# Kernel tuning notes

Measured on AMD Instinct MI355X. Metric: run time of the kernel, lower is better.

Reference implementation:

```python
import jax, jax.numpy as jnp
import numpy as np

B, I_LEN, Q_LEN, H = 256, 256, 64, 512
MID, G, FLAT_OUT = 512, 1, 1024


def setup_inputs() -> dict:
    key = jax.random.key(0)
    ks = jax.random.split(key, 20)
    s = lambda k, sh: jax.random.normal(k, sh, dtype=jnp.float32) * 0.02
    inp = {
        'i_batch': jax.random.normal(ks[0], (B, I_LEN, H), dtype=jnp.float32),
        'q_batch': jax.random.normal(ks[1], (B, Q_LEN, H), dtype=jnp.float32),
        'i_mask': jax.random.bernoulli(ks[2], 0.1, (B, 1, 1, I_LEN)),
        'q_mask': jax.random.bernoulli(ks[3], 0.1, (B, 1, 1, Q_LEN)),
        # l_flatten (applied to i_feat) params
        'lf_w1': s(ks[4], (H, MID)), 'lf_b1': jnp.zeros((MID,), jnp.float32),
        'lf_w2': s(ks[5], (MID, G)), 'lf_b2': jnp.zeros((G,), jnp.float32),
        'lf_wm': s(ks[6], (H * G, FLAT_OUT)), 'lf_bm': jnp.zeros((FLAT_OUT,), jnp.float32),
        # i_flatten (applied to l_feat) params
        'if_w1': s(ks[7], (H, MID)), 'if_b1': jnp.zeros((MID,), jnp.float32),
        'if_w2': s(ks[8], (MID, G)), 'if_b2': jnp.zeros((G,), jnp.float32),
        'if_wm': s(ks[9], (H * G, FLAT_OUT)), 'if_bm': jnp.zeros((FLAT_OUT,), jnp.float32),
        # fh_h: Linear(1024, 512)
        'fh_w': s(ks[10], (FLAT_OUT, 512)), 'fh_b': jnp.zeros((512,), jnp.float32),
    }
    return inp


def _qkv_attention(query, key, value, mask):
    # query [B,Lq,H], key/value [B,Lk,H], mask [B,1,1,Lk] (True = pad)
    d_k = query.shape[-1]
    scores = jnp.einsum('bqh,bkh->bqk', query, key) / jnp.sqrt(jnp.asarray(d_k, query.dtype))
    scores = jnp.where(mask[:, 0], jnp.asarray(-65504.0, scores.dtype), scores)
    p_attn = jax.nn.softmax(scores, axis=-1)
    return jnp.einsum('bqk,bkh->bqh', p_attn, value)


def _att_flat(x, x_mask, w1, b1, w2, b2, wm, bm):
    # x [B,L,H], x_mask [B,1,1,L]
    att = jnp.maximum(x @ w1 + b1, 0.0) @ w2 + b2           # [B,L,G]
    att = jnp.where(x_mask[:, 0, 0, :, None], -1e9, att)
    att = jax.nn.softmax(att, axis=1)
    pooled = jnp.einsum('blg,blh->bgh', att, x).reshape(x.shape[0], -1)  # [B,G*H]
    return pooled @ wm + bm, att[..., 0]                    # att.squeeze() with G=1


def reference(i_batch, q_batch, i_mask, q_mask,
              lf_w1, lf_b1, lf_w2, lf_b2, lf_wm, lf_bm,
              if_w1, if_b1, if_w2, if_b2, if_wm, if_bm,
              fh_w, fh_b):
    i_feat = _qkv_attention(i_batch, q_batch, q_batch, q_mask)   # [B,I_LEN,H]
    i_feat, i_weight = _att_flat(i_feat, i_mask, lf_w1, lf_b1, lf_w2, lf_b2, lf_wm, lf_bm)
    l_feat = _qkv_attention(q_batch, i_batch, i_batch, i_mask)   # [B,Q_LEN,H]
    l_feat, _ = _att_flat(l_feat, q_mask, if_w1, if_b1, if_w2, if_b2, if_wm, if_bm)
    out = (l_feat + i_feat) @ fh_w + fh_b                        # [B,512]
    return out, i_weight
```

## Files before the change

### kernel.cpp

```cpp
#include <hip/hip_runtime.h>
#include <math.h>


#define SCALE 0.04419417382415922f

typedef __attribute__((ext_vector_type(8))) short short8;
typedef __attribute__((ext_vector_type(4))) float floatx4;

__device__ __forceinline__ unsigned short f2bf(float x) {
  unsigned u = __float_as_uint(x);
  unsigned r = u + 0x7FFFu + ((u >> 16) & 1u);
  return (unsigned short)(r >> 16);
}
__device__ __forceinline__ float bf2f(unsigned short h) {
  return __uint_as_float(((unsigned)h) << 16);
}
__device__ __forceinline__ unsigned pk2(float a, float b) {
  return (unsigned)f2bf(a) | ((unsigned)f2bf(b) << 16);
}

__device__ __forceinline__ float wave_max(float v) {
#pragma unroll
  for (int o = 32; o > 0; o >>= 1) v = fmaxf(v, __shfl_xor(v, o, 64));
  return v;
}
__device__ __forceinline__ float wave_sum(float v) {
#pragma unroll
  for (int o = 32; o > 0; o >>= 1) v += __shfl_xor(v, o, 64);
  return v;
}

#define GLD_LDS16(gptr, lptr)                                             \
  __builtin_amdgcn_global_load_lds(                                       \
      (const __attribute__((address_space(1))) void*)(gptr),              \
      (__attribute__((address_space(3))) void*)(lptr), 16, 0, 0)

__global__ __launch_bounds__(256) void k_prep(
    const float* __restrict__ ib, const float* __restrict__ qb,
    const float* __restrict__ lf_w1, const float* __restrict__ if_w1,
    const float* __restrict__ lf_wm, const float* __restrict__ if_wm,
    const float* __restrict__ fh_w, unsigned short* __restrict__ ib_bf,
    unsigned short* __restrict__ ibT, unsigned short* __restrict__ qb_bf,
    unsigned short* __restrict__ qbT, unsigned short* __restrict__ w1t_lf,
    unsigned short* __restrict__ w1t_if, unsigned short* __restrict__ wcat_t,
    unsigned short* __restrict__ fh_wt) {
  __shared__ __align__(16) char smem[128 * 136 * 2];
  const int idx = blockIdx.x, t = threadIdx.x;

  if (idx < 512) {
    float(*T)[65] = (float(*)[65])smem;
    const float* src;
    unsigned short* dst;
    int N, ds, koff, k0, n0;
    if (idx < 64) {
      src = lf_w1; dst = w1t_lf; N = 512; ds = 512; koff = 0;
      k0 = (idx & 7) * 64; n0 = (idx >> 3) * 64;
    } else if (idx < 128) {
      int l = idx - 64;
      src = if_w1; dst = w1t_if; N = 512; ds = 512; koff = 0;
      k0 = (l & 7) * 64; n0 = (l >> 3) * 64;
    } else if (idx < 256) {
      int l = idx - 128;
      src = lf_wm; dst = wcat_t; N = 1024; ds = 1024; koff = 0;
      k0 = (l & 7) * 64; n0 = (l >> 3) * 64;
    } else if (idx < 384) {
      int l = idx - 256;
      src = if_wm; dst = wcat_t; N = 1024; ds = 1024; koff = 512;
      k0 = (l & 7) * 64; n0 = (l >> 3) * 64;
    } else {
      int l = idx - 384;
      src = fh_w; dst = fh_wt; N = 512; ds = 1024; koff = 0;
      k0 = (l & 15) * 64; n0 = (l >> 4) * 64;
    }
#pragma unroll
    for (int i = 0; i < 16; i++) {
      int e = t + i * 256, r = e >> 6, c = e & 63;
      T[r][c] = src[(size_t)(k0 + r) * N + n0 + c];
    }
    __syncthreads();
#pragma unroll
    for (int i = 0; i < 8; i++) {
      int e = t + i * 256, r = e >> 5, c2 = (e & 31) * 2;
      *(unsigned*)&dst[(size_t)(n0 + r) * ds + koff + k0 + c2] =
          pk2(T[c2][r], T[c2 + 1][r]);
    }
  } else if (idx < 2560) {
    int j = idx - 512;
    int b = j >> 3, tok0 = ((j >> 2) & 1) * 128, h0 = (j & 3) * 128;
    unsigned short* Tb = (unsigned short*)smem;
    const float* src = ib + ((size_t)b * 256 + tok0) * 512 + h0;
#pragma unroll
    for (int i = 0; i < 16; i++) {
      int e = t + i * 256, tok = e >> 5, h4 = (e & 31) * 4;
      float4 v = *(const float4*)&src[(size_t)tok * 512 + h4];
      uint2 p;
      p.x = pk2(v.x, v.y);
      p.y = pk2(v.z, v.w);
      *(uint2*)&Tb[tok * 136 + h4] = p;
    }
    __syncthreads();
    unsigned short* dbf = ib_bf + ((size_t)b * 256 + tok0) * 512 + h0;
#pragma unroll
    for (int i = 0; i < 8; i++) {
      int e = t + i * 256, tok = e >> 4, hc = (e & 15) * 8;
      *(uint4*)&dbf[(size_t)tok * 512 + hc] = *(const uint4*)&Tb[tok * 136 + hc];
    }
    unsigned short* dT = ibT + ((size_t)b * 512 + h0) * 256 + tok0;
#pragma unroll
    for (int i = 0; i < 8; i++) {
      int e = t + i * 256, h = e >> 4, tc = (e & 15) * 8;
      unsigned x0 = Tb[(tc + 0) * 136 + h], x1 = Tb[(tc + 1) * 136 + h];
      unsigned x2 = Tb[(tc + 2) * 136 + h], x3 = Tb[(tc + 3) * 136 + h];
      unsigned x4 = Tb[(tc + 4) * 136 + h], x5 = Tb[(tc + 5) * 136 + h];
      unsigned x6 = Tb[(tc + 6) * 136 + h], x7 = Tb[(tc + 7) * 136 + h];
      uint4 v;
      v.x = x0 | (x1 << 16);
      v.y = x2 | (x3 << 16);
      v.z = x4 | (x5 << 16);
      v.w = x6 | (x7 << 16);
      *(uint4*)&dT[(size_t)h * 256 + tc] = v;
    }
  } else {
    int j = idx - 2560;
    int b = j >> 3, h0 = (j & 7) * 64;
    float(*T)[65] = (float(*)[65])smem;
    const float* src = qb + (size_t)b * 64 * 512;
    unsigned short* dbf = qb_bf + (size_t)b * 64 * 512;
    unsigned short* dT = qbT + (size_t)b * 512 * 64;
#pragma unroll
    for (int i = 0; i < 16; i++) {
      int e = t + i * 256, r = e >> 6, c = e & 63;
      T[r][c] = src[(size_t)r * 512 + h0 + c];
    }
    __syncthreads();
#pragma unroll
    for (int i = 0; i < 8; i++) {
      int e = t + i * 256, r = e >> 5, c2 = (e & 31) * 2;
      *(unsigned*)&dbf[(size_t)r * 512 + h0 + c2] = pk2(T[r][c2], T[r][c2 + 1]);
    }
#pragma unroll
    for (int i = 0; i < 8; i++) {
      int e = t + i * 256, h = e >> 5, r2 = (e & 31) * 2;
      *(unsigned*)&dT[(size_t)(h0 + h) * 64 + r2] = pk2(T[r2][h], T[r2 + 1][h]);
    }
  }
}

__global__ __launch_bounds__(256) void k_scores_f(
    const unsigned short* __restrict__ ibf, const unsigned short* __restrict__ qbf,
    const int* __restrict__ imask, const int* __restrict__ qmask,
    unsigned short* __restrict__ P1, unsigned short* __restrict__ P2,
    float* __restrict__ psum) {
  __shared__ unsigned short As[64 * 64];
  __shared__ unsigned short Bs[128 * 64];
  __shared__ __align__(16) unsigned short X[128 * 72];
  const int b = blockIdx.y, ic = blockIdx.x, i0 = ic * 128;
  const int t = threadIdx.x, w = t >> 6, lane = t & 63, c = lane & 15, qq = lane >> 4;

  floatx4 acc[4][2];
#pragma unroll
  for (int ti = 0; ti < 4; ti++)
#pragma unroll
    for (int tj = 0; tj < 2; tj++) acc[ti][tj] = (floatx4){0.f, 0.f, 0.f, 0.f};

  for (int k0 = 0; k0 < 512; k0 += 64) {
#pragma unroll
    for (int i = 0; i < 2; i++) {
      int s = i * 256 + t, row = s >> 3, src = (s & 7) ^ (row & 7);
      GLD_LDS16(qbf + ((size_t)b * 64 + row) * 512 + k0 + src * 8,
                &As[(i * 256 + w * 64) * 8]);
    }
#pragma unroll
    for (int i = 0; i < 4; i++) {
      int s = i * 256 + t, row = s >> 3, src = (s & 7) ^ (row & 7);
      GLD_LDS16(ibf + ((size_t)b * 256 + i0 + row) * 512 + k0 + src * 8,
                &Bs[(i * 256 + w * 64) * 8]);
    }
    __syncthreads();
#pragma unroll
    for (int kk = 0; kk < 2; kk++) {
      short8 a[4], bb[2];
#pragma unroll
      for (int ti = 0; ti < 4; ti++)
        a[ti] = *(const short8*)&As[(ti * 16 + c) * 64 + ((kk * 4 + qq) ^ (c & 7)) * 8];
#pragma unroll
      for (int tj = 0; tj < 2; tj++)
        bb[tj] = *(const short8*)&Bs[(w * 32 + tj * 16 + c) * 64 + ((kk * 4 + qq) ^ (c & 7)) * 8];
#pragma unroll
      for (int ti = 0; ti < 4; ti++)
#pragma unroll
        for (int tj = 0; tj < 2; tj++)
          acc[ti][tj] = __builtin_amdgcn_mfma_f32_16x16x32_bf16(a[ti], bb[tj], acc[ti][tj], 0, 0, 0);
    }
    __syncthreads();
  }

  const int il0 = w * 32 + c;
  int imsk0 = imask[b * 256 + i0 + il0];
  int imsk1 = imask[b * 256 + i0 + il0 + 16];
  int qm[4][4];
#pragma unroll
  for (int ti = 0; ti < 4; ti++)
#pragma unroll
    for (int rr = 0; rr < 4; rr++) qm[ti][rr] = qmask[b * 64 + ti * 16 + qq * 4 + rr];

#pragma unroll
  for (int ti = 0; ti < 4; ti++)
#pragma unroll
    for (int rr = 0; rr < 4; rr++) {
      int qv = ti * 16 + qq * 4 + rr;
      float e0 = imsk0 ? 0.f : __expf(acc[ti][0][rr] * SCALE);
      float e1 = imsk1 ? 0.f : __expf(acc[ti][1][rr] * SCALE);
      X[qv * 136 + il0] = f2bf(e0);
      X[qv * 136 + il0 + 16] = f2bf(e1);
      float s = e0 + e1;
#pragma unroll
      for (int o = 1; o <= 8; o <<= 1) s += __shfl_xor(s, o, 64);
      if (c == 0) psum[((size_t)(b * 64 + qv)) * 8 + ic * 4 + w] = s;
    }
  __syncthreads();
#pragma unroll
  for (int i = 0; i < 4; i++) {
    int e2 = t + i * 256, qv = e2 >> 4, g = e2 & 15;
    *(uint4*)&P2[((size_t)b * 64 + qv) * 256 + i0 + g * 8] = *(const uint4*)&X[qv * 136 + g * 8];
  }
  __syncthreads();

#pragma unroll
  for (int tj = 0; tj < 2; tj++) {
    float ev[4][4];
    float s1 = 0.f;
#pragma unroll
    for (int ti = 0; ti < 4; ti++)
#pragma unroll
      for (int rr = 0; rr < 4; rr++) {
        ev[ti][rr] = qm[ti][rr] ? 0.f : __expf(acc[ti][tj][rr] * SCALE);
        s1 += ev[ti][rr];
      }
    s1 += __shfl_xor(s1, 16, 64);
    s1 += __shfl_xor(s1, 32, 64);
    float inv = 1.f / s1;
    int il = il0 + tj * 16;
#pragma unroll
    for (int ti = 0; ti < 4; ti++)
#pragma unroll
      for (int rr = 0; rr < 4; rr++)
        X[il * 72 + ti * 16 + qq * 4 + rr] = f2bf(ev[ti][rr] * inv);
  }
  __syncthreads();
#pragma unroll
  for (int i = 0; i < 4; i++) {
    int e2 = t + i * 256, il = e2 >> 3, g = e2 & 7;
    *(uint4*)&P1[((size_t)b * 256 + i0 + il) * 64 + g * 8] = *(const uint4*)&X[il * 72 + g * 8];
  }
}

__global__ __launch_bounds__(256) void k_p2norm(unsigned short* __restrict__ P2,
                                                const float* __restrict__ psum) {
  const int row = blockIdx.x * 4 + (threadIdx.x >> 6);
  const int lane = threadIdx.x & 63;
  const float* ps = psum + (size_t)row * 8;
  float s = ps[0] + ps[1] + ps[2] + ps[3] + ps[4] + ps[5] + ps[6] + ps[7];
  float inv = 1.f / s;
  uint2* p = (uint2*)&P2[(size_t)row * 256 + lane * 4];
  uint2 v = *p;
  uint2 o;
  o.x = pk2(bf2f((unsigned short)(v.x & 0xffff)) * inv,
            bf2f((unsigned short)(v.x >> 16)) * inv);
  o.y = pk2(bf2f((unsigned short)(v.y & 0xffff)) * inv,
            bf2f((unsigned short)(v.y >> 16)) * inv);
  *p = o;
}

__global__ __launch_bounds__(256) void k_av1(const unsigned short* __restrict__ P1,
                                             const unsigned short* __restrict__ qbT,
                                             unsigned short* __restrict__ ifeat) {
  __shared__ unsigned short As[128 * 64];
  __shared__ unsigned short Bs[128 * 64];
  const int b = blockIdx.y, m0 = (blockIdx.x >> 2) * 128, n0 = (blockIdx.x & 3) * 128;
  const int t = threadIdx.x, w = t >> 6, lane = t & 63, c = lane & 15, q = lane >> 4;
  const int wm = w >> 1, wn = w & 1;
#pragma unroll
  for (int i = 0; i < 4; i++) {
    int s = i * 256 + t, row = s >> 3, src = (s & 7) ^ (row & 7);
    GLD_LDS16(P1 + ((size_t)b * 256 + m0 + row) * 64 + src * 8, &As[(i * 256 + w * 64) * 8]);
  }
#pragma unroll
  for (int i = 0; i < 4; i++) {
    int s = i * 256 + t, row = s >> 3, src = (s & 7) ^ (row & 7);
    GLD_LDS16(qbT + ((size_t)b * 512 + n0 + row) * 64 + src * 8, &Bs[(i * 256 + w * 64) * 8]);
  }
  __syncthreads();
  floatx4 acc[4][4];
#pragma unroll
  for (int ti = 0; ti < 4; ti++)
#pragma unroll
    for (int tj = 0; tj < 4; tj++) acc[ti][tj] = (floatx4){0.f, 0.f, 0.f, 0.f};
#pragma unroll
  for (int kk = 0; kk < 2; kk++) {
    short8 a[4], bb[4];
#pragma unroll
    for (int ti = 0; ti < 4; ti++)
      a[ti] = *(const short8*)&As[(wm * 64 + ti * 16 + c) * 64 + ((kk * 4 + q) ^ (c & 7)) * 8];
#pragma unroll
    for (int tj = 0; tj < 4; tj++)
      bb[tj] = *(const short8*)&Bs[(wn * 64 + tj * 16 + c) * 64 + ((kk * 4 + q) ^ (c & 7)) * 8];
#pragma unroll
    for (int ti = 0; ti < 4; ti++)
#pragma unroll
      for (int tj = 0; tj < 4; tj++)
        acc[ti][tj] = __builtin_amdgcn_mfma_f32_16x16x32_bf16(a[ti], bb[tj], acc[ti][tj], 0, 0, 0);
  }
#pragma unroll
  for (int ti = 0; ti < 4; ti++)
#pragma unroll
    for (int rr = 0; rr < 4; rr++) {
      int m = m0 + wm * 64 + ti * 16 + q * 4 + rr;
      unsigned short* op = ifeat + ((size_t)b * 256 + m) * 512 + n0 + wn * 64;
#pragma unroll
      for (int tj = 0; tj < 4; tj++) op[tj * 16 + c] = f2bf(acc[ti][tj][rr]);
    }
}

__global__ __launch_bounds__(256) void k_av2(const unsigned short* __restrict__ P2,
                                             const unsigned short* __restrict__ ibT,
                                             unsigned short* __restrict__ lfeat) {
  __shared__ unsigned short As[64 * 64];
  __shared__ unsigned short Bs[128 * 64];
  const int b = blockIdx.y, n0 = blockIdx.x * 128;
  const int t = threadIdx.x, w = t >> 6, lane = t & 63, c = lane & 15, q = lane >> 4;
  const int wm = w >> 1, wn = w & 1;
  floatx4 acc[2][4];
#pragma unroll
  for (int ti = 0; ti < 2; ti++)
#pragma unroll
    for (int tj = 0; tj < 4; tj++) acc[ti][tj] = (floatx4){0.f, 0.f, 0.f, 0.f};

  for (int kc = 0; kc < 256; kc += 64) {
#pragma unroll
    for (int i = 0; i < 2; i++) {
      int s = i * 256 + t, row = s >> 3, src = (s & 7) ^ (row & 7);
      GLD_LDS16(P2 + ((size_t)b * 64 + row) * 256 + kc + src * 8, &As[(i * 256 + w * 64) * 8]);
    }
#pragma unroll
    for (int i = 0; i < 4; i++) {
      int s = i * 256 + t, row = s >> 3, src = (s & 7) ^ (row & 7);
      GLD_LDS16(ibT + ((size_t)b * 512 + n0 + row) * 256 + kc + src * 8,
                &Bs[(i * 256 + w * 64) * 8]);
    }
    __syncthreads();
#pragma unroll
    for (int kk = 0; kk < 2; kk++) {
      short8 a[2], bb[4];
#pragma unroll
      for (int ti = 0; ti < 2; ti++)
        a[ti] = *(const short8*)&As[(wm * 32 + ti * 16 + c) * 64 + ((kk * 4 + q) ^ (c & 7)) * 8];
#pragma unroll
      for (int tj = 0; tj < 4; tj++)
        bb[tj] = *(const short8*)&Bs[(wn * 64 + tj * 16 + c) * 64 + ((kk * 4 + q) ^ (c & 7)) * 8];
#pragma unroll
      for (int ti = 0; ti < 2; ti++)
#pragma unroll
        for (int tj = 0; tj < 4; tj++)
          acc[ti][tj] = __builtin_amdgcn_mfma_f32_16x16x32_bf16(a[ti], bb[tj], acc[ti][tj], 0, 0, 0);
    }
    __syncthreads();
  }
#pragma unroll
  for (int ti = 0; ti < 2; ti++)
#pragma unroll
    for (int rr = 0; rr < 4; rr++) {
      int m = wm * 32 + ti * 16 + q * 4 + rr;
      unsigned short* op = lfeat + ((size_t)b * 64 + m) * 512 + n0 + wn * 64;
#pragma unroll
      for (int tj = 0; tj < 4; tj++) op[tj * 16 + c] = f2bf(acc[ti][tj][rr]);
    }
}

__global__ __launch_bounds__(256) void k_logits_part(
    const unsigned short* __restrict__ X, const unsigned short* __restrict__ W1t,
    const float* __restrict__ b1, const float* __restrict__ w2,
    float* __restrict__ outp, int M) {
  __shared__ unsigned short As[128 * 64];
  __shared__ unsigned short Bs[128 * 64];
  __shared__ float red[2][128];
  const int t = threadIdx.x, w = t >> 6, lane = t & 63;
  const int wm = w >> 1, wn = w & 1, c = lane & 15, q = lane >> 4;
  const int idx = blockIdx.x;
  const int m_tile = (idx & 7) + ((idx >> 5) << 3), nc = (idx >> 3) & 3;
  const int m0 = m_tile * 128, n0 = nc * 128;

  floatx4 acc[4][4];
#pragma unroll
  for (int ti = 0; ti < 4; ti++)
#pragma unroll
    for (int tj = 0; tj < 4; tj++) acc[ti][tj] = (floatx4){0.f, 0.f, 0.f, 0.f};

  for (int k0 = 0; k0 < 512; k0 += 64) {
#pragma unroll
    for (int it = 0; it < 4; it++) {
      int s = it * 256 + t, row = s >> 3, src = (s & 7) ^ (row & 7);
      GLD_LDS16(X + (size_t)(m0 + row) * 512 + k0 + src * 8, &As[(it * 256 + w * 64) * 8]);
      GLD_LDS16(W1t + (size_t)(n0 + row) * 512 + k0 + src * 8, &Bs[(it * 256 + w * 64) * 8]);
    }
    __syncthreads();
#pragma unroll
    for (int kk = 0; kk < 2; kk++) {
      short8 a[4], bb[4];
#pragma unroll
      for (int ti = 0; ti < 4; ti++)
        a[ti] = *(const short8*)&As[(wm * 64 + ti * 16 + c) * 64 + ((kk * 4 + q) ^ (c & 7)) * 8];
#pragma unroll
      for (int tj = 0; tj < 4; tj++)
        bb[tj] = *(const short8*)&Bs[(wn * 64 + tj * 16 + c) * 64 + ((kk * 4 + q) ^ (c & 7)) * 8];
#pragma unroll
      for (int ti = 0; ti < 4; ti++)
#pragma unroll
        for (int tj = 0; tj < 4; tj++)
          acc[ti][tj] = __builtin_amdgcn_mfma_f32_16x16x32_bf16(a[ti], bb[tj], acc[ti][tj], 0, 0, 0);
    }
    __syncthreads();
  }
  float partial[4][4] = {};
#pragma unroll
  for (int tj = 0; tj < 4; tj++) {
    int n = n0 + wn * 64 + tj * 16 + c;
    float bia = b1[n], wwv = w2[n];
#pragma unroll
    for (int ti = 0; ti < 4; ti++)
#pragma unroll
      for (int r = 0; r < 4; r++)
        partial[ti][r] += fmaxf(acc[ti][tj][r] + bia, 0.f) * wwv;
  }
#pragma unroll
  for (int msk = 1; msk <= 8; msk <<= 1)
#pragma unroll
    for (int ti = 0; ti < 4; ti++)
#pragma unroll
      for (int r = 0; r < 4; r++)
        partial[ti][r] += __shfl_xor(partial[ti][r], msk, 64);
  if (c == 0) {
#pragma unroll
    for (int ti = 0; ti < 4; ti++)
#pragma unroll
      for (int r = 0; r < 4; r++)
        red[wn][wm * 64 + ti * 16 + q * 4 + r] = partial[ti][r];
  }
  __syncthreads();
  if (t < 128) outp[(size_t)nc * M + m0 + t] = red[0][t] + red[1][t];
}

__global__ __launch_bounds__(256) void k_attsoft_i(const float* __restrict__ lp,
                                                   const int* __restrict__ imask,
                                                   float* __restrict__ att,
                                                   float* __restrict__ iw_out) {
  __shared__ float red[4];
  const int b = blockIdx.x, t = threadIdx.x;
  const int i = b * 256 + t;
  float x = lp[i] + lp[65536 + i] + lp[131072 + i] + lp[196608 + i];
  float v = imask[i] ? -1e9f : x;
  float wm = wave_max(v);
  if ((t & 63) == 0) red[t >> 6] = wm;
  __syncthreads();
  float mx = fmaxf(fmaxf(red[0], red[1]), fmaxf(red[2], red[3]));
  __syncthreads();
  float e = __expf(v - mx);
  float wsum = wave_sum(e);
  if ((t & 63) == 0) red[t >> 6] = wsum;
  __syncthreads();
  float s = red[0] + red[1] + red[2] + red[3];
  float p = e / s;
  att[i] = p;
  iw_out[i] = p;
}

__global__ __launch_bounds__(64) void k_attsoft_l(const float* __restrict__ lp,
                                                  const int* __restrict__ qmask,
                                                  float* __restrict__ att) {
  const int b = blockIdx.x, t = threadIdx.x;
  const int i = b * 64 + t;
  float x = lp[i] + lp[16384 + i] + lp[32768 + i] + lp[49152 + i];
  float v = qmask[i] ? -1e9f : x;
  float mx = wave_max(v);
  float e = __expf(v - mx);
  float s = wave_sum(e);
  att[i] = e / s;
}

__global__ __launch_bounds__(256) void k_pooled(const unsigned short* __restrict__ X,
                                                const float* __restrict__ att, int L,
                                                unsigned short* __restrict__ out,
                                                int ooff) {
  __shared__ float ar[256];
  const int b = blockIdx.x, t = threadIdx.x;
  if (t < L) ar[t] = att[b * L + t];
  __syncthreads();
  float a0 = 0.f, a1 = 0.f;
  const unsigned short* Xb = X + (size_t)b * L * 512 + 2 * t;
  for (int l = 0; l < L; l++) {
    unsigned u = *(const unsigned*)&Xb[(size_t)l * 512];
    float a = ar[l];
    a0 += a * bf2f((unsigned short)(u & 0xffff));
    a1 += a * bf2f((unsigned short)(u >> 16));
  }
  *(unsigned*)&out[(size_t)b * 1024 + ooff + 2 * t] = pk2(a0, a1);
}

__global__ __launch_bounds__(256) void k_egemm(const unsigned short* __restrict__ X,
                                               const unsigned short* __restrict__ Wt,
                                               const float* __restrict__ biasA,
                                               const float* __restrict__ biasB,
                                               float* __restrict__ outf,
                                               unsigned short* __restrict__ outbf,
                                               int N, int K) {
  __shared__ unsigned short As[64 * 64];
  __shared__ unsigned short Bs[64 * 64];
  const int n0 = blockIdx.x * 64, m0 = blockIdx.y * 64;
  const int t = threadIdx.x, w = t >> 6, lane = t & 63, c = lane & 15, q = lane >> 4;
  const int wm = w >> 1, wn = w & 1;
  floatx4 acc[2][2];
#pragma unroll
  for (int ti = 0; ti < 2; ti++)
#pragma unroll
    for (int tj = 0; tj < 2; tj++) acc[ti][tj] = (floatx4){0.f, 0.f, 0.f, 0.f};

  for (int k0 = 0; k0 < K; k0 += 64) {
#pragma unroll
    for (int i = 0; i < 2; i++) {
      int s = i * 256 + t, row = s >> 3, src = (s & 7) ^ (row & 7);
      GLD_LDS16(X + (size_t)(m0 + row) * K + k0 + src * 8, &As[(i * 256 + w * 64) * 8]);
      GLD_LDS16(Wt + (size_t)(n0 + row) * K + k0 + src * 8, &Bs[(i * 256 + w * 64) * 8]);
    }
    __syncthreads();
#pragma unroll
    for (int kk = 0; kk < 2; kk++) {
      short8 a[2], bb[2];
#pragma unroll
      for (int ti = 0; ti < 2; ti++)
        a[ti] = *(const short8*)&As[(wm * 32 + ti * 16 + c) * 64 + ((kk * 4 + q) ^ (c & 7)) * 8];
#pragma unroll
      for (int tj = 0; tj < 2; tj++)
        bb[tj] = *(const short8*)&Bs[(wn * 32 + tj * 16 + c) * 64 + ((kk * 4 + q) ^ (c & 7)) * 8];
#pragma unroll
      for (int ti = 0; ti < 2; ti++)
#pragma unroll
        for (int tj = 0; tj < 2; tj++)
          acc[ti][tj] = __builtin_amdgcn_mfma_f32_16x16x32_bf16(a[ti], bb[tj], acc[ti][tj], 0, 0, 0);
    }
    __syncthreads();
  }
#pragma unroll
  for (int tj = 0; tj < 2; tj++) {
    int n = n0 + wn * 32 + tj * 16 + c;
    float bias = biasA[n] + (biasB ? biasB[n] : 0.f);
#pragma unroll
    for (int ti = 0; ti < 2; ti++)
#pragma unroll
      for (int rr = 0; rr < 4; rr++) {
        int m = m0 + wm * 32 + ti * 16 + q * 4 + rr;
        float v = acc[ti][tj][rr] + bias;
        if (outbf) outbf[(size_t)m * N + n] = f2bf(v);
        else outf[(size_t)m * N + n] = v;
      }
  }
}

extern "C" void kernel_launch(void* const* d_in, const int* in_sizes, int n_in,
                              void* d_out, int out_size, void* d_ws, size_t ws_size,
                              hipStream_t stream) {
  const float* ib = (const float*)d_in[0];
  const float* qb = (const float*)d_in[1];
  const int* imask = (const int*)d_in[2];
  const int* qmask = (const int*)d_in[3];
  const float* lf_w1 = (const float*)d_in[4];
  const float* lf_b1 = (const float*)d_in[5];
  const float* lf_w2 = (const float*)d_in[6];
  const float* lf_wm = (const float*)d_in[8];
  const float* lf_bm = (const float*)d_in[9];
  const float* if_w1 = (const float*)d_in[10];
  const float* if_b1 = (const float*)d_in[11];
  const float* if_w2 = (const float*)d_in[12];
  const float* if_wm = (const float*)d_in[14];
  const float* if_bm = (const float*)d_in[15];
  const float* fh_w = (const float*)d_in[16];
  const float* fh_b = (const float*)d_in[17];
  float* out = (float*)d_out;

  float* lp_i = (float*)d_ws;
  float* lp_l = lp_i + 262144;
  float* att_i = lp_l + 65536;
  float* att_l = att_i + 65536;
  float* psum = att_l + 16384;
  unsigned short* P1 = (unsigned short*)(psum + 131072);
  unsigned short* P2 = P1 + 4194304;
  unsigned short* ib_bf = P2 + 4194304;
  unsigned short* qb_bf = ib_bf + 33554432;
  unsigned short* qbT = qb_bf + 8388608;
  unsigned short* ibT = qbT + 8388608;
  unsigned short* w1t_lf = ibT + 33554432;
  unsigned short* w1t_if = w1t_lf + 262144;
  unsigned short* wcat_t = w1t_if + 262144;
  unsigned short* fh_wt = wcat_t + 1048576;
  unsigned short* pooled_bf = fh_wt + 524288;
  unsigned short* F_bf = pooled_bf + 262144;
  unsigned short* ifeat = ib_bf;
  unsigned short* lfeat = qb_bf;

  k_prep<<<4608, 256, 0, stream>>>(ib, qb, lf_w1, if_w1, lf_wm, if_wm, fh_w,
                                   ib_bf, ibT, qb_bf, qbT, w1t_lf, w1t_if,
                                   wcat_t, fh_wt);

  k_scores_f<<<dim3(2, 256), 256, 0, stream>>>(ib_bf, qb_bf, imask, qmask, P1, P2, psum);
  k_p2norm<<<4096, 256, 0, stream>>>(P2, psum);
  k_av1<<<dim3(8, 256), 256, 0, stream>>>(P1, qbT, ifeat);
  k_av2<<<dim3(4, 256), 256, 0, stream>>>(P2, ibT, lfeat);

  k_logits_part<<<2048, 256, 0, stream>>>(ifeat, w1t_lf, lf_b1, lf_w2, lp_i, 65536);
  k_logits_part<<<512, 256, 0, stream>>>(lfeat, w1t_if, if_b1, if_w2, lp_l, 16384);
  k_attsoft_i<<<256, 256, 0, stream>>>(lp_i, imask, att_i, out + 131072);
  k_attsoft_l<<<256, 64, 0, stream>>>(lp_l, qmask, att_l);
  k_pooled<<<256, 256, 0, stream>>>(ifeat, att_i, 256, pooled_bf, 0);
  k_pooled<<<256, 256, 0, stream>>>(lfeat, att_l, 64, pooled_bf, 512);

  k_egemm<<<dim3(16, 4), 256, 0, stream>>>(pooled_bf, wcat_t, lf_bm, if_bm,
                                           nullptr, F_bf, 1024, 1024);
  k_egemm<<<dim3(8, 4), 256, 0, stream>>>(F_bf, fh_wt, fh_b, nullptr,
                                          out, nullptr, 512, 1024);
}
```

Baseline: 463.2 us.

## Fuse softmax normalization into AV2 epilogue and XOR-swizzle prep transpose LDS

Drops the separate P2 normalization kernel. k_av2 now multiplies its accumulators by the reciprocal of the summed partial row sums in its epilogue, which saves a launch and a full read/write pass over P2. The input-batch transpose in k_prep also swaps its padded LDS tile for an XOR-swizzled unpadded layout, to cut bank conflicts and LDS footprint. Because normalization now happens after the bf16 matmul rather than on the bf16 probabilities, rounding changes slightly; a leftover dummy read stays in the transpose loop.

Measured after the change: 457.7 us. No clear change (-1.2%).

```diff
diff --git a/kernel.cpp b/kernel.cpp
--- a/kernel.cpp
+++ b/kernel.cpp
@@ -44,7 +44,7 @@
     unsigned short* __restrict__ qbT, unsigned short* __restrict__ w1t_lf,
     unsigned short* __restrict__ w1t_if, unsigned short* __restrict__ wcat_t,
     unsigned short* __restrict__ fh_wt) {
-  __shared__ __align__(16) char smem[128 * 136 * 2];
+  __shared__ __align__(16) char smem[128 * 128 * 2];
   const int idx = blockIdx.x, t = threadIdx.x;
 
   if (idx < 512) {
@@ -96,28 +96,35 @@
       uint2 p;
       p.x = pk2(v.x, v.y);
       p.y = pk2(v.z, v.w);
-      *(uint2*)&Tb[tok * 136 + h4] = p;
+      int col = ((((h4 >> 3) ^ (tok >> 3)) & 15) << 3) | (h4 & 7);
+      *(uint2*)&Tb[tok * 128 + col] = p;
     }
     __syncthreads();
     unsigned short* dbf = ib_bf + ((size_t)b * 256 + tok0) * 512 + h0;
 #pragma unroll
     for (int i = 0; i < 8; i++) {
-      int e = t + i * 256, tok = e >> 4, hc = (e & 15) * 8;
-      *(uint4*)&dbf[(size_t)tok * 512 + hc] = *(const uint4*)&Tb[tok * 136 + hc];
+      int e = t + i * 256, tok = e >> 4, g = e & 15;
+      int sg = (g ^ (tok >> 3)) & 15;
+      *(uint4*)&dbf[(size_t)tok * 512 + g * 8] = *(const uint4*)&Tb[tok * 128 + sg * 8];
     }
     unsigned short* dT = ibT + ((size_t)b * 512 + h0) * 256 + tok0;
 #pragma unroll
     for (int i = 0; i < 8; i++) {
       int e = t + i * 256, h = e >> 4, tc = (e & 15) * 8;
-      unsigned x0 = Tb[(tc + 0) * 136 + h], x1 = Tb[(tc + 1) * 136 + h];
-      unsigned x2 = Tb[(tc + 2) * 136 + h], x3 = Tb[(tc + 3) * 136 + h];
-      unsigned x4 = Tb[(tc + 4) * 136 + h], x5 = Tb[(tc + 5) * 136 + h];
-      unsigned x6 = Tb[(tc + 6) * 136 + h], x7 = Tb[(tc + 7) * 136 + h];
+      int hg = h >> 3, ho = h & 7;
+      unsigned x0 = Tb[(tc + 0) * 128 + ((((tc + 0) >> 3) ^ hg & 15) << 3 ^ ((hg ^ ((tc + 0) >> 3)) & 15) << 3) + 0];
+      (void)x0;
+      unsigned y[8];
+#pragma unroll
+      for (int k = 0; k < 8; k++) {
+        int r = tc + k;
+        y[k] = Tb[r * 128 + (((hg ^ (r >> 3)) & 15) << 3) + ho];
+      }
       uint4 v;
-      v.x = x0 | (x1 << 16);
-      v.y = x2 | (x3 << 16);
-      v.z = x4 | (x5 << 16);
-      v.w = x6 | (x7 << 16);
+      v.x = y[0] | (y[1] << 16);
+      v.y = y[2] | (y[3] << 16);
+      v.z = y[4] | (y[5] << 16);
+      v.w = y[6] | (y[7] << 16);
       *(uint4*)&dT[(size_t)h * 256 + tc] = v;
     }
   } else {
@@ -255,23 +262,6 @@
   }
 }
 
-__global__ __launch_bounds__(256) void k_p2norm(unsigned short* __restrict__ P2,
-                                                const float* __restrict__ psum) {
-  const int row = blockIdx.x * 4 + (threadIdx.x >> 6);
-  const int lane = threadIdx.x & 63;
-  const float* ps = psum + (size_t)row * 8;
-  float s = ps[0] + ps[1] + ps[2] + ps[3] + ps[4] + ps[5] + ps[6] + ps[7];
-  float inv = 1.f / s;
-  uint2* p = (uint2*)&P2[(size_t)row * 256 + lane * 4];
-  uint2 v = *p;
-  uint2 o;
-  o.x = pk2(bf2f((unsigned short)(v.x & 0xffff)) * inv,
-            bf2f((unsigned short)(v.x >> 16)) * inv);
-  o.y = pk2(bf2f((unsigned short)(v.y & 0xffff)) * inv,
-            bf2f((unsigned short)(v.y >> 16)) * inv);
-  *p = o;
-}
-
 __global__ __launch_bounds__(256) void k_av1(const unsigned short* __restrict__ P1,
                                              const unsigned short* __restrict__ qbT,
                                              unsigned short* __restrict__ ifeat) {
@@ -324,6 +314,7 @@
 
 __global__ __launch_bounds__(256) void k_av2(const unsigned short* __restrict__ P2,
                                              const unsigned short* __restrict__ ibT,
+                                             const float* __restrict__ psum,
                                              unsigned short* __restrict__ lfeat) {
   __shared__ unsigned short As[64 * 64];
   __shared__ unsigned short Bs[128 * 64];
@@ -371,9 +362,12 @@
 #pragma unroll
     for (int rr = 0; rr < 4; rr++) {
       int m = wm * 32 + ti * 16 + q * 4 + rr;
+      const float* ps = psum + ((size_t)(b * 64 + m)) * 8;
+      float s = ps[0] + ps[1] + ps[2] + ps[3] + ps[4] + ps[5] + ps[6] + ps[7];
+      float inv = 1.f / s;
       unsigned short* op = lfeat + ((size_t)b * 64 + m) * 512 + n0 + wn * 64;
 #pragma unroll
-      for (int tj = 0; tj < 4; tj++) op[tj * 16 + c] = f2bf(acc[ti][tj][rr]);
+      for (int tj = 0; tj < 4; tj++) op[tj * 16 + c] = f2bf(acc[ti][tj][rr] * inv);
     }
 }
 
@@ -611,9 +605,8 @@
                                    wcat_t, fh_wt);
 
   k_scores_f<<<dim3(2, 256), 256, 0, stream>>>(ib_bf, qb_bf, imask, qmask, P1, P2, psum);
-  k_p2norm<<<4096, 256, 0, stream>>>(P2, psum);
   k_av1<<<dim3(8, 256), 256, 0, stream>>>(P1, qbT, ifeat);
-  k_av2<<<dim3(4, 256), 256, 0, stream>>>(P2, ibT, lfeat);
+  k_av2<<<dim3(4, 256), 256, 0, stream>>>(P2, ibT, psum, lfeat);
 
   k_logits_part<<<2048, 256, 0, stream>>>(ifeat, w1t_lf, lf_b1, lf_w2, lp_i, 65536);
   k_logits_part<<<512, 256, 0, stream>>>(lfeat, w1t_if, if_b1, if_w2, lp_l, 16384);
```
